# Performance work log

Measured on AMD Instinct MI355X. Metric: run time of the kernel, lower is better.

The kernel has to match this reference:

```python
import jax, jax.numpy as jnp
import numpy as np

B, N, C = 8192, 64, 256  # batch, num_nodes, cells; depth=2


def setup_inputs() -> dict:
    key = jax.random.key(0)
    ks = jax.random.split(key, 9)
    scale1 = 1.0  # fan_in = 1
    scaleC = 1.0 / np.sqrt(C)
    return {
        "Q": jax.random.normal(ks[0], (B, N), dtype=jnp.float32),
        "Y": jax.random.normal(ks[1], (B, N), dtype=jnp.float32),
        # stacked per-node MLP params: Linear(1,C) -> ReLU -> Linear(C,C) -> ReLU -> Linear(C,1)
        "W1": jax.random.normal(ks[2], (N, 1, C), dtype=jnp.float32) * scale1,
        "b1": jax.random.normal(ks[3], (N, C), dtype=jnp.float32) * scale1,
        "W2": jax.random.normal(ks[4], (N, C, C), dtype=jnp.float32) * scaleC,
        "b2": jax.random.normal(ks[5], (N, C), dtype=jnp.float32) * scaleC,
        "W3": jax.random.normal(ks[6], (N, C, 1), dtype=jnp.float32) * scaleC,
        "b3": jax.random.normal(ks[7], (N, 1), dtype=jnp.float32) * scaleC,
        "bias_0": jnp.ones((1, 1), dtype=jnp.float32),
    }


def reference(Q, Y, W1, b1, W2, b2, W3, b3, bias_0):
    s = Q * Y  # [B, N], per-node scalar input s_i = q_i * y_i
    # layer 1: scalar -> C  (W1[n,0,:] broadcast over batch)
    h = jax.nn.relu(s[:, :, None] * W1[None, :, 0, :] + b1[None])  # [B, N, C]
    # layer 2: C -> C, batched over nodes
    h = jax.nn.relu(jnp.einsum("bnc,ncd->bnd", h, W2) + b2[None])  # [B, N, C]
    # layer 3: C -> scalar
    z_i = jnp.einsum("bnc,nc->bn", h, W3[:, :, 0]) + b3[None, :, 0]  # [B, N]
    z_0 = bias_0 - jnp.sum(s, axis=-1, keepdims=True)  # [B, 1]
    z = jnp.concatenate([z_0, z_i], axis=-1)  # [B, N+1]
    z = jax.nn.softmax(z, axis=-1)
    return jax.nn.relu(z)
```

## Files before the change

kernel.cpp:

```cpp
#include <hip/hip_runtime.h>
#include <hip/hip_bf16.h>


typedef unsigned int u32;
typedef __fp16 fp16x2 __attribute__((ext_vector_type(2)));
union U32H { u32 u; fp16x2 h; };

__device__ __forceinline__ u32 pkh(float a, float b) {
    U32H cv; cv.h = __builtin_amdgcn_cvt_pkrtz(a, b); return cv.u;
}
__device__ __forceinline__ float dot2f(u32 a, u32 b, float c) {
    float d;
    asm("v_dot2_f32_f16 %0, %1, %2, %3" : "=v"(d) : "v"(a), "v"(b), "v"(c));
    return d;
}

__global__ __launch_bounds__(256) void prep(
    const float* __restrict__ Q, const float* __restrict__ Y,
    const float* __restrict__ W1, const float* __restrict__ b1,
    float* __restrict__ S, float* __restrict__ knots, int* __restrict__ perm)
{
    __shared__ float ts[64][65];
    __shared__ float key[256];
    __shared__ int   idx[256];

    const int blk = blockIdx.x;
    const int tid = threadIdx.x;

    if (blk < 128) {
        const int b0 = blk << 6;
        #pragma unroll
        for (int jj = 0; jj < 16; jj++) {
            int i = tid + (jj << 8);
            int r = i >> 6, c = i & 63;
            ts[r][c] = Q[(size_t)(b0 + r) * 64 + c] * Y[(size_t)(b0 + r) * 64 + c];
        }
        __syncthreads();
        #pragma unroll
        for (int jj = 0; jj < 16; jj++) {
            int i = tid + (jj << 8);
            int nn = i >> 6, bb = i & 63;
            S[((size_t)nn << 13) + b0 + bb] = ts[bb][nn];
        }
    } else {
        const int n = blk - 128;
        {
            float w = W1[n * 256 + tid];
            float b = b1[n * 256 + tid];
            key[tid] = -b / w;
            idx[tid] = tid;
        }
        __syncthreads();
        for (int k = 2; k <= 256; k <<= 1) {
            for (int j = k >> 1; j > 0; j >>= 1) {
                int p = tid ^ j;
                if (p > tid) {
                    float a = key[tid], c = key[p];
                    bool up = ((tid & k) == 0);
                    if (up ? (a > c) : (a < c)) {
                        int ia = idx[tid];
                        key[tid] = c; idx[tid] = idx[p];
                        key[p] = a; idx[p] = ia;
                    }
                }
                __syncthreads();
            }
        }
        knots[n * 256 + tid] = key[tid];
        perm[n * 256 + tid]  = idx[tid];
    }
}

__global__ __launch_bounds__(256) void build_sort(
    const float* __restrict__ W1, const float* __restrict__ b1,
    const float* __restrict__ W2, const float* __restrict__ b2,
    const int* __restrict__ perm, const float* __restrict__ S,
    const float* __restrict__ knots,
    uint2* __restrict__ table, uint2* __restrict__ sorted)
{
    __shared__ float w1s[256], b1s[256];
    __shared__ int   pm[256];
    __shared__ float part[16][16][8];
    __shared__ u32   hist[257];

    const int blk = blockIdx.x;
    const int tid = threadIdx.x;
    const int lane = tid & 63;

    if (blk < 512) {
        const int n    = blk >> 3;
        const int strip= blk & 7;
        const int prl  = tid & 15;
        const int seg  = tid >> 4;
        const int prg  = (strip << 4) + prl;
        const int d0   = prg << 1;

        w1s[tid] = W1[n * 256 + tid];
        b1s[tid] = b1[n * 256 + tid];
        pm[tid]  = perm[n * 256 + tid];
        __syncthreads();

        const float* W2n = W2 + ((size_t)n << 16);
        float2 vreg[16];

        {
            float ba0 = 0.f, bc0 = 0.f, ba1 = 0.f, bc1 = 0.f;
            float da0 = 0.f, dc0 = 0.f, da1 = 0.f, dc1 = 0.f;
            #pragma unroll
            for (int i = 0; i < 16; ++i) {
                int   kj = pm[(seg << 4) + i];
                float w  = w1s[kj];
                float bb = b1s[kj];
                float2 v = *reinterpret_cast<const float2*>(&W2n[kj * 256 + d0]);
                vreg[i] = v;
                if (w < 0.f) {
                    ba0 = fmaf(v.x, w, ba0); bc0 = fmaf(v.x, bb, bc0);
                    ba1 = fmaf(v.y, w, ba1); bc1 = fmaf(v.y, bb, bc1);
                }
                float aw = fabsf(w);
                float cs = (w > 0.f) ? bb : -bb;
                da0 = fmaf(v.x, aw, da0); dc0 = fmaf(v.x, cs, dc0);
                da1 = fmaf(v.y, aw, da1); dc1 = fmaf(v.y, cs, dc1);
            }
            float* p = part[seg][prl];
            p[0] = ba0; p[1] = bc0; p[2] = ba1; p[3] = bc1;
            p[4] = da0; p[5] = dc0; p[6] = da1; p[7] = dc1;
        }
        __syncthreads();

        if (tid < 16) {
            const int pr = tid;
            float sa0 = 0.f, sc0 = 0.f, sa1 = 0.f, sc1 = 0.f;
            #pragma unroll
            for (int sg = 0; sg < 16; ++sg) {
                const float* p = part[sg][pr];
                sa0 += p[0]; sc0 += p[1]; sa1 += p[2]; sc1 += p[3];
            }
            const int dd = ((strip << 4) + pr) << 1;
            sc0 += b2[n * 256 + dd];
            sc1 += b2[n * 256 + dd + 1];
            table[(size_t)n * 257 * 128 + ((strip << 4) + pr)] =
                make_uint2(pkh(sa0, sa1), pkh(sc0, sc1));
            float ra0 = sa0, rc0 = sc0, ra1 = sa1, rc1 = sc1;
            #pragma unroll
            for (int sg = 0; sg < 16; ++sg) {
                float* p = part[sg][pr];
                float t4 = p[4], t5 = p[5], t6 = p[6], t7 = p[7];
                p[0] = ra0; p[1] = rc0; p[2] = ra1; p[3] = rc1;
                ra0 += t4; rc0 += t5; ra1 += t6; rc1 += t7;
            }
        }
        __syncthreads();

        {
            const float* p = part[seg][prl];
            float a0 = p[0], c0 = p[1], a1 = p[2], c1 = p[3];
            uint2* trow = table + (size_t)n * 257 * 128 + prg;
            #pragma unroll
            for (int i = 0; i < 16; ++i) {
                int   j  = (seg << 4) + i;
                int   kj = pm[j];
                float w  = w1s[kj];
                float bb = b1s[kj];
                float2 v = vreg[i];
                float aw = fabsf(w);
                float cs = (w > 0.f) ? bb : -bb;
                a0 = fmaf(v.x, aw, a0); c0 = fmaf(v.x, cs, c0);
                a1 = fmaf(v.y, aw, a1); c1 = fmaf(v.y, cs, c1);
                trow[(size_t)(j + 1) * 128] = make_uint2(pkh(a0, a1), pkh(c0, c1));
            }
        }
    } else {
        const int t = blk - 512;
        const int n = t >> 2;
        const int q = t & 3;

        float* kn = w1s;
        kn[tid] = knots[n * 256 + tid];
        hist[tid] = 0;
        if (tid == 0) hist[256] = 0;
        __syncthreads();

        const float* Sn = S + ((size_t)n << 13) + (q << 11);
        float sv[8]; int iv[8];
        #pragma unroll
        for (int j = 0; j < 8; ++j) {
            const float s = Sn[tid + (j << 8)];
            sv[j] = s;
            int I = 0;
            #pragma unroll
            for (int step = 128; step >= 1; step >>= 1)
                if (kn[I + step - 1] < s) I += step;
            if (I < 256 && kn[I] < s) I += 1;
            iv[j] = I;
            atomicAdd(&hist[I], 1u);
        }
        __syncthreads();

        if (tid < 64) {
            int base = tid << 2;
            u32 h0 = hist[base], h1 = hist[base + 1], h2 = hist[base + 2], h3 = hist[base + 3];
            u32 lsum = h0 + h1 + h2 + h3;
            u32 run = lsum;
            #pragma unroll
            for (int off = 1; off < 64; off <<= 1) {
                u32 tt = __shfl_up(run, off, 64);
                if (lane >= off) run += tt;
            }
            u32 excl = run - lsum;
            hist[base]     = excl;
            hist[base + 1] = excl + h0;
            hist[base + 2] = excl + h0 + h1;
            hist[base + 3] = excl + h0 + h1 + h2;
            if (tid == 63) hist[256] = excl + lsum;
        }
        __syncthreads();

        uint2* dst = sorted + ((size_t)n << 13) + (q << 11);
        #pragma unroll
        for (int j = 0; j < 8; ++j) {
            u32 pos = atomicAdd(&hist[iv[j]], 1u);
            u32 bglob = (u32)((q << 11) + tid + (j << 8));
            dst[pos] = make_uint2(__float_as_uint(sv[j]), ((u32)iv[j] << 13) | bglob);
        }
    }
}

__global__ __launch_bounds__(256) void eval_nodes(
    const uint2* __restrict__ sorted, const uint2* __restrict__ table,
    const float* __restrict__ W3, const float* __restrict__ b3,
    float* __restrict__ Z)
{
    __shared__ u32 w3p[128];

    const int n   = blockIdx.x;
    const int c0  = blockIdx.y << 8;
    const int tid = threadIdx.x;

    if (tid < 128)
        w3p[tid] = pkh(W3[n * 256 + (tid << 1)], W3[n * 256 + (tid << 1) + 1]);
    __syncthreads();

    const uint2 ent = sorted[((size_t)n << 13) + c0 + tid];
    const float s   = __uint_as_float(ent.x);
    const int   I   = (int)(ent.y >> 13);
    const int   bl  = (int)(ent.y & 8191u);

    U32H s2; s2.u = pkh(s, s);
    const fp16x2 z2 = (fp16x2)0;

    const uint4* row = reinterpret_cast<const uint4*>(
        table + (size_t)((u32)n * 257 + I) * 128);

    float acc0 = 0.f, acc1 = 0.f;
    #pragma unroll 4
    for (int q = 0; q < 64; ++q) {
        uint4 v = row[q];
        uint2 w = reinterpret_cast<const uint2*>(w3p)[q];
        U32H a01{v.x}, b01{v.y}, a23{v.z}, b23{v.w};
        U32H h01, h23;
        h01.h = __builtin_elementwise_max(a01.h * s2.h + b01.h, z2);
        h23.h = __builtin_elementwise_max(a23.h * s2.h + b23.h, z2);
        acc0 = dot2f(h01.u, w.x, acc0);
        acc1 = dot2f(h23.u, w.y, acc1);
    }
    Z[((size_t)n << 13) + bl] = acc0 + acc1 + b3[n];
}

__global__ __launch_bounds__(256) void softmax_rows(
    const float* __restrict__ Q, const float* __restrict__ Y,
    const float* __restrict__ Z, const float* __restrict__ bias0,
    float* __restrict__ out)
{
    __shared__ float ts[64][65];
    const int b0   = blockIdx.x << 6;
    const int tid  = threadIdx.x;
    const int lane = tid & 63;
    const int wv   = tid >> 6;

    #pragma unroll
    for (int jj = 0; jj < 16; jj++) {
        int idx = tid + (jj << 8);
        int nn = idx >> 6, bb = idx & 63;
        ts[bb][nn] = Z[((size_t)nn << 13) + b0 + bb];
    }
    __syncthreads();

    const float bias = bias0[0];
    #pragma unroll 2
    for (int r = 0; r < 16; ++r) {
        const int row = (wv << 4) + r;
        const int b   = b0 + row;

        float s = Q[(size_t)b * 64 + lane] * Y[(size_t)b * 64 + lane];
        float ssum = s;
        #pragma unroll
        for (int mask = 32; mask >= 1; mask >>= 1) ssum += __shfl_xor(ssum, mask, 64);
        const float z0 = bias - ssum;

        float zl = ts[row][lane];
        float mx = zl;
        #pragma unroll
        for (int mask = 32; mask >= 1; mask >>= 1) mx = fmaxf(mx, __shfl_xor(mx, mask, 64));
        mx = fmaxf(mx, z0);

        float el = expf(zl - mx);
        float e0 = expf(z0 - mx);
        float den = el;
        #pragma unroll
        for (int mask = 32; mask >= 1; mask >>= 1) den += __shfl_xor(den, mask, 64);
        den += e0;
        const float inv = 1.0f / den;

        out[(size_t)b * 65 + 1 + lane] = el * inv;
        if (lane == 0) out[(size_t)b * 65] = e0 * inv;
    }
}

extern "C" void kernel_launch(void* const* d_in, const int* in_sizes, int n_in,
                              void* d_out, int out_size, void* d_ws, size_t ws_size,
                              hipStream_t stream)
{
    const float* Q     = (const float*)d_in[0];
    const float* Y     = (const float*)d_in[1];
    const float* W1    = (const float*)d_in[2];
    const float* b1    = (const float*)d_in[3];
    const float* W2    = (const float*)d_in[4];
    const float* b2    = (const float*)d_in[5];
    const float* W3    = (const float*)d_in[6];
    const float* b3    = (const float*)d_in[7];
    const float* bias0 = (const float*)d_in[8];
    float* out = (float*)d_out;

    char* ws = (char*)d_ws;
    uint2* table  = (uint2*)ws;
    float* S      = (float*)(ws + 16842752);
    float* Z      = (float*)(ws + 18939904);
    float* knots  = (float*)(ws + 21037056);
    int*   perm   = (int*)  (ws + 21102592);
    uint2* sorted = (uint2*)(ws + 21168128);

    prep<<<192, 256, 0, stream>>>(Q, Y, W1, b1, S, knots, perm);
    build_sort<<<768, 256, 0, stream>>>(W1, b1, W2, b2, perm, S, knots, table, sorted);
    eval_nodes<<<dim3(64, 32), 256, 0, stream>>>(sorted, table, W3, b3, Z);
    softmax_rows<<<128, 256, 0, stream>>>(Q, Y, Z, bias0, out);
}
```

Baseline: 64.77 us.

## Collapse per-interval layer-2 units into affine sums plus sparse crossing entries

In the table build, each layer-2 output unit in each knot interval is now classified as always active, always dead, or crossing zero within that interval. Active units are folded with W3 into a single affine coefficient pair per interval strip. Only crossing units are stored as fp32 entries that need a per-sample ReLU. The evaluation kernel then sums 8 partial pairs and loops over the few crossing entries instead of all 256 fp16 units, which cuts memory reads and ALU work. In exchange the workspace grows, the build gains per-interval DPP reductions and scans, and the eval loop has a data-dependent trip count that can diverge within a wavefront.

```diff
diff --git a/kernel.cpp b/kernel.cpp
--- a/kernel.cpp
+++ b/kernel.cpp
@@ -3,16 +3,18 @@
 
 
 typedef unsigned int u32;
-typedef __fp16 fp16x2 __attribute__((ext_vector_type(2)));
-union U32H { u32 u; fp16x2 h; };
-
-__device__ __forceinline__ u32 pkh(float a, float b) {
-    U32H cv; cv.h = __builtin_amdgcn_cvt_pkrtz(a, b); return cv.u;
-}
-__device__ __forceinline__ float dot2f(u32 a, u32 b, float c) {
-    float d;
-    asm("v_dot2_f32_f16 %0, %1, %2, %3" : "=v"(d) : "v"(a), "v"(b), "v"(c));
-    return d;
+
+__device__ __forceinline__ float row_reduce16(float x) {
+    int v;
+    v = __builtin_amdgcn_update_dpp(0, __float_as_int(x), 0xB1, 0xF, 0xF, false);
+    x += __int_as_float(v);
+    v = __builtin_amdgcn_update_dpp(0, __float_as_int(x), 0x4E, 0xF, 0xF, false);
+    x += __int_as_float(v);
+    v = __builtin_amdgcn_update_dpp(0, __float_as_int(x), 0x124, 0xF, 0xF, false);
+    x += __int_as_float(v);
+    v = __builtin_amdgcn_update_dpp(0, __float_as_int(x), 0x128, 0xF, 0xF, false);
+    x += __int_as_float(v);
+    return x;
 }
 
 __global__ __launch_bounds__(256) void prep(
@@ -74,11 +76,12 @@
 __global__ __launch_bounds__(256) void build_sort(
     const float* __restrict__ W1, const float* __restrict__ b1,
     const float* __restrict__ W2, const float* __restrict__ b2,
-    const int* __restrict__ perm, const float* __restrict__ S,
-    const float* __restrict__ knots,
-    uint2* __restrict__ table, uint2* __restrict__ sorted)
+    const float* __restrict__ W3, const int* __restrict__ perm,
+    const float* __restrict__ S, const float* __restrict__ knots,
+    float4* __restrict__ entries, float2* __restrict__ AccP,
+    unsigned char* __restrict__ cnt8, uint2* __restrict__ sorted)
 {
-    __shared__ float w1s[256], b1s[256];
+    __shared__ float w1s[256], b1s[256], kns[256];
     __shared__ int   pm[256];
     __shared__ float part[16][16][8];
     __shared__ u32   hist[257];
@@ -97,9 +100,12 @@
 
         w1s[tid] = W1[n * 256 + tid];
         b1s[tid] = b1[n * 256 + tid];
+        kns[tid] = knots[n * 256 + tid];
         pm[tid]  = perm[n * 256 + tid];
         __syncthreads();
 
+        const float w30 = W3[n * 256 + d0];
+        const float w31 = W3[n * 256 + d0 + 1];
         const float* W2n = W2 + ((size_t)n << 16);
         float2 vreg[16];
 
@@ -139,8 +145,36 @@
             const int dd = ((strip << 4) + pr) << 1;
             sc0 += b2[n * 256 + dd];
             sc1 += b2[n * 256 + dd + 1];
-            table[(size_t)n * 257 * 128 + ((strip << 4) + pr)] =
-                make_uint2(pkh(sa0, sa1), pkh(sc0, sc1));
+
+            float k0 = kns[0];
+            float hLo0 = (sa0 != 0.f) ? -sa0 : sc0;
+            float hHi0 = fmaf(sa0, k0, sc0);
+            float hLo1 = (sa1 != 0.f) ? -sa1 : sc1;
+            float hHi1 = fmaf(sa1, k0, sc1);
+            bool act0 = hLo0 > 0.f && hHi0 > 0.f, drp0 = hLo0 <= 0.f && hHi0 <= 0.f;
+            bool act1 = hLo1 > 0.f && hHi1 > 0.f, drp1 = hLo1 <= 0.f && hHi1 <= 0.f;
+            bool cr0 = !act0 && !drp0, cr1 = !act1 && !drp1;
+            float As = (act0 ? w30 * sa0 : 0.f) + (act1 ? w31 * sa1 : 0.f);
+            float Bs = (act0 ? w30 * sc0 : 0.f) + (act1 ? w31 * sc1 : 0.f);
+            As = row_reduce16(As); Bs = row_reduce16(Bs);
+            u32 cx = (u32)cr0 + (u32)cr1;
+            u32 incl = cx, t;
+            t = __shfl_up(incl, 1, 64); if (pr >= 1) incl += t;
+            t = __shfl_up(incl, 2, 64); if (pr >= 2) incl += t;
+            t = __shfl_up(incl, 4, 64); if (pr >= 4) incl += t;
+            t = __shfl_up(incl, 8, 64); if (pr >= 8) incl += t;
+            u32 excl = incl - cx;
+            u32 tot  = __shfl(incl, 15, 64);
+            size_t ib = (size_t)(n * 257 + 0) * 8 + strip;
+            size_t eb = ib * 32;
+            u32 off = excl;
+            if (cr0) { entries[eb + off] = make_float4(sa0, sc0, w30, 0.f); off++; }
+            if (cr1) { entries[eb + off] = make_float4(sa1, sc1, w31, 0.f); }
+            if (pr == 0) {
+                AccP[ib] = make_float2(As, Bs);
+                cnt8[ib] = (unsigned char)tot;
+            }
+
             float ra0 = sa0, rc0 = sc0, ra1 = sa1, rc1 = sc1;
             #pragma unroll
             for (int sg = 0; sg < 16; ++sg) {
@@ -155,8 +189,7 @@
         {
             const float* p = part[seg][prl];
             float a0 = p[0], c0 = p[1], a1 = p[2], c1 = p[3];
-            uint2* trow = table + (size_t)n * 257 * 128 + prg;
-            #pragma unroll
+            #pragma unroll 4
             for (int i = 0; i < 16; ++i) {
                 int   j  = (seg << 4) + i;
                 int   kj = pm[j];
@@ -167,7 +200,40 @@
                 float cs = (w > 0.f) ? bb : -bb;
                 a0 = fmaf(v.x, aw, a0); c0 = fmaf(v.x, cs, c0);
                 a1 = fmaf(v.y, aw, a1); c1 = fmaf(v.y, cs, c1);
-                trow[(size_t)(j + 1) * 128] = make_uint2(pkh(a0, a1), pkh(c0, c1));
+
+                float lo = kns[j];
+                float hLo0 = fmaf(a0, lo, c0), hLo1 = fmaf(a1, lo, c1);
+                float hHi0, hHi1;
+                if (j < 255) {
+                    float hi = kns[j + 1];
+                    hHi0 = fmaf(a0, hi, c0); hHi1 = fmaf(a1, hi, c1);
+                } else {
+                    hHi0 = (a0 != 0.f) ? a0 : c0;
+                    hHi1 = (a1 != 0.f) ? a1 : c1;
+                }
+                bool act0 = hLo0 > 0.f && hHi0 > 0.f, drp0 = hLo0 <= 0.f && hHi0 <= 0.f;
+                bool act1 = hLo1 > 0.f && hHi1 > 0.f, drp1 = hLo1 <= 0.f && hHi1 <= 0.f;
+                bool cr0 = !act0 && !drp0, cr1 = !act1 && !drp1;
+                float As = (act0 ? w30 * a0 : 0.f) + (act1 ? w31 * a1 : 0.f);
+                float Bs = (act0 ? w30 * c0 : 0.f) + (act1 ? w31 * c1 : 0.f);
+                As = row_reduce16(As); Bs = row_reduce16(Bs);
+                u32 cx = (u32)cr0 + (u32)cr1;
+                u32 incl = cx, t;
+                t = __shfl_up(incl, 1, 64); if (prl >= 1) incl += t;
+                t = __shfl_up(incl, 2, 64); if (prl >= 2) incl += t;
+                t = __shfl_up(incl, 4, 64); if (prl >= 4) incl += t;
+                t = __shfl_up(incl, 8, 64); if (prl >= 8) incl += t;
+                u32 excl = incl - cx;
+                u32 tot  = __shfl(incl, (lane & ~15) + 15, 64);
+                size_t ib = (size_t)(n * 257 + (j + 1)) * 8 + strip;
+                size_t eb = ib * 32;
+                u32 off = excl;
+                if (cr0) { entries[eb + off] = make_float4(a0, c0, w30, 0.f); off++; }
+                if (cr1) { entries[eb + off] = make_float4(a1, c1, w31, 0.f); }
+                if (prl == 0) {
+                    AccP[ib] = make_float2(As, Bs);
+                    cnt8[ib] = (unsigned char)tot;
+                }
             }
         }
     } else {
@@ -227,44 +293,41 @@
 }
 
 __global__ __launch_bounds__(256) void eval_nodes(
-    const uint2* __restrict__ sorted, const uint2* __restrict__ table,
-    const float* __restrict__ W3, const float* __restrict__ b3,
-    float* __restrict__ Z)
+    const uint2* __restrict__ sorted, const float4* __restrict__ entries,
+    const float2* __restrict__ AccP, const unsigned char* __restrict__ cnt8,
+    const float* __restrict__ b3, float* __restrict__ Z)
 {
-    __shared__ u32 w3p[128];
-
     const int n   = blockIdx.x;
     const int c0  = blockIdx.y << 8;
     const int tid = threadIdx.x;
-
-    if (tid < 128)
-        w3p[tid] = pkh(W3[n * 256 + (tid << 1)], W3[n * 256 + (tid << 1) + 1]);
-    __syncthreads();
 
     const uint2 ent = sorted[((size_t)n << 13) + c0 + tid];
     const float s   = __uint_as_float(ent.x);
     const int   I   = (int)(ent.y >> 13);
     const int   bl  = (int)(ent.y & 8191u);
 
-    U32H s2; s2.u = pkh(s, s);
-    const fp16x2 z2 = (fp16x2)0;
-
-    const uint4* row = reinterpret_cast<const uint4*>(
-        table + (size_t)((u32)n * 257 + I) * 128);
-
-    float acc0 = 0.f, acc1 = 0.f;
-    #pragma unroll 4
-    for (int q = 0; q < 64; ++q) {
-        uint4 v = row[q];
-        uint2 w = reinterpret_cast<const uint2*>(w3p)[q];
-        U32H a01{v.x}, b01{v.y}, a23{v.z}, b23{v.w};
-        U32H h01, h23;
-        h01.h = __builtin_elementwise_max(a01.h * s2.h + b01.h, z2);
-        h23.h = __builtin_elementwise_max(a23.h * s2.h + b23.h, z2);
-        acc0 = dot2f(h01.u, w.x, acc0);
-        acc1 = dot2f(h23.u, w.y, acc1);
-    }
-    Z[((size_t)n << 13) + bl] = acc0 + acc1 + b3[n];
+    const size_t base = (size_t)(n * 257 + I) * 8;
+
+    float A = 0.f, B = 0.f;
+    #pragma unroll
+    for (int k = 0; k < 8; ++k) {
+        float2 t = AccP[base + k];
+        A += t.x; B += t.y;
+    }
+    float z = fmaf(A, s, B);
+
+    const uint2 cc = *reinterpret_cast<const uint2*>(&cnt8[base]);
+    #pragma unroll
+    for (int st = 0; st < 8; ++st) {
+        u32 c = (st < 4) ? ((cc.x >> (st * 8)) & 0xFFu)
+                         : ((cc.y >> ((st - 4) * 8)) & 0xFFu);
+        const float4* ep = entries + ((base + st) << 5);
+        for (u32 jj = 0; jj < c; ++jj) {
+            float4 e = ep[jj];
+            z = fmaf(e.z, fmaxf(fmaf(e.x, s, e.y), 0.f), z);
+        }
+    }
+    Z[((size_t)n << 13) + bl] = z + b3[n];
 }
 
 __global__ __launch_bounds__(256) void softmax_rows(
@@ -333,15 +396,18 @@
     float* out = (float*)d_out;
 
     char* ws = (char*)d_ws;
-    uint2* table  = (uint2*)ws;
-    float* S      = (float*)(ws + 16842752);
-    float* Z      = (float*)(ws + 18939904);
-    float* knots  = (float*)(ws + 21037056);
-    int*   perm   = (int*)  (ws + 21102592);
-    uint2* sorted = (uint2*)(ws + 21168128);
+    float4* entries      = (float4*)ws;
+    float2* AccP         = (float2*)(ws + 67371008);
+    unsigned char* cnt8  = (unsigned char*)(ws + 68423680);
+    float* S             = (float*)(ws + 68555264);
+    float* Z             = (float*)(ws + 70652416);
+    float* knots         = (float*)(ws + 72749568);
+    int*   perm          = (int*)  (ws + 72815104);
+    uint2* sorted        = (uint2*)(ws + 72880640);
 
     prep<<<192, 256, 0, stream>>>(Q, Y, W1, b1, S, knots, perm);
-    build_sort<<<768, 256, 0, stream>>>(W1, b1, W2, b2, perm, S, knots, table, sorted);
-    eval_nodes<<<dim3(64, 32), 256, 0, stream>>>(sorted, table, W3, b3, Z);
+    build_sort<<<768, 256, 0, stream>>>(W1, b1, W2, b2, W3, perm, S, knots,
+                                        entries, AccP, cnt8, sorted);
+    eval_nodes<<<dim3(64, 32), 256, 0, stream>>>(sorted, entries, AccP, cnt8, b3, Z);
     softmax_rows<<<128, 256, 0, stream>>>(Q, Y, Z, bias0, out);
 }
```

After: 55.42 us, median of 2. 1.17x faster.
